# Optimization experiments

Hardware: AMD Instinct MI355X
Metric: run time of the kernel (lower is better)

## Reference

```python
import jax, jax.numpy as jnp
import numpy as np

FEATURE_DIM = 128
VALUE_DIM = 128


def setup_inputs() -> dict:
    key = jax.random.key(0)
    k1, k2, k3 = jax.random.split(key, 3)
    BH, S = 32, 4096
    q = jax.random.normal(k1, (BH, S, FEATURE_DIM), dtype=jnp.float32)
    k = jax.random.normal(k2, (BH, S, FEATURE_DIM), dtype=jnp.float32)
    v = jax.random.normal(k3, (BH, S, VALUE_DIM), dtype=jnp.float32)
    return {"q": q, "k": k, "v": v, "chunk_size": 128}


def reference(q, k, v, chunk_size):
    # q,k: [BH,S,F]; v: [BH,S,V]. Chunked fast-weight linear-attention scan:
    # out_t = q_t . (sum_{s<=t} k_s (x) v_s) / t
    BH, S, F = q.shape
    V = v.shape[-1]
    C = max(1, int(chunk_size))
    assert S % C == 0, "seq_len must be divisible by chunk_size for this reference"
    n_chunks = S // C
    # [n_chunks, BH, C, dim] for lax.scan over chunks
    qc = q.reshape(BH, n_chunks, C, F).transpose(1, 0, 2, 3)
    kc = k.reshape(BH, n_chunks, C, F).transpose(1, 0, 2, 3)
    vc = v.reshape(BH, n_chunks, C, V).transpose(1, 0, 2, 3)

    w0 = jnp.zeros((BH, F, V), dtype=q.dtype)

    def step(w_state, inputs):
        qi, ki, vi = inputs  # [BH,C,F], [BH,C,F], [BH,C,V]
        kv = jnp.einsum('bnf,bnv->bnfv', ki, vi)          # [BH,C,F,V]
        w_prefix = jnp.cumsum(kv, axis=1) + w_state[:, None]  # inclusive prefix sums
        out = jnp.einsum('bnf,bnfv->bnv', qi, w_prefix)    # [BH,C,V]
        return w_prefix[:, -1], out

    _, outs = jax.lax.scan(step, w0, (qc, kc, vc))
    out = outs.transpose(1, 0, 2, 3).reshape(BH, S, V)
    inv_counts = 1.0 / jnp.arange(1, S + 1, dtype=q.dtype)
    return out * inv_counts[None, :, None]
```

## Files before the change

kernel.cpp:

```cpp
#include <hip/hip_runtime.h>


typedef _Float16 f16;
typedef __attribute__((ext_vector_type(4))) _Float16 f16x4;
typedef __attribute__((ext_vector_type(8))) _Float16 f16x8;
typedef __attribute__((ext_vector_type(4))) float f32x4;
typedef __attribute__((ext_vector_type(16))) float f32x16;
typedef __attribute__((ext_vector_type(4))) float fv4;

#define MFMA16(a, b, c) __builtin_amdgcn_mfma_f32_16x16x32_f16((a), (b), (c), 0, 0, 0)
#define MFMA32(a, b, c) __builtin_amdgcn_mfma_f32_32x32x16_f16((a), (b), (c), 0, 0, 0)

__device__ __forceinline__ int swzb(int row, int col) {
  int s = (row ^ (row >> 3)) & 7;
  return (row << 8) + ((col << 1) ^ (s << 4));
}

__device__ __forceinline__ f16x8 frag32(const f16* lds, int row, int kk, int lane) {
  int c0 = (kk << 4) + ((lane >> 5) << 3);
  return *(const f16x8*)((const char*)lds + swzb(row, c0));
}

__device__ __forceinline__ int rowf(int r, int g) {
  return (r & 3) + ((r >> 2) << 3) + (g << 2);
}

__global__ __launch_bounds__(512, 1)
void ttr_pt(const float* __restrict__ k, const float* __restrict__ v,
            f16* __restrict__ pt) {
  __shared__ f16 kT[128 * 128];
  __shared__ f16 vT[128 * 128];
  const int tid = threadIdx.x, lane = tid & 63, wave = tid >> 6;
  const int bh = blockIdx.x >> 5, c = blockIdx.x & 31;
  const float* kg = k + ((size_t)bh * 4096 + c * 128) * 128;
  const float* vg = v + ((size_t)bh * 4096 + c * 128) * 128;
  const int f0 = (tid & 31) << 2;
#pragma unroll
  for (int p = 0; p < 8; ++p) {
    int s = (p << 4) + (tid >> 5);
    fv4 xk = *(const fv4*)(kg + s * 128 + f0);
    fv4 xv = *(const fv4*)(vg + s * 128 + f0);
#pragma unroll
    for (int e = 0; e < 4; ++e) {
      *(f16*)((char*)kT + swzb(f0 + e, s)) = (f16)xk[e];
      *(f16*)((char*)vT + swzb(f0 + e, s)) = (f16)xv[e];
    }
  }
  __syncthreads();
  const int l31 = lane & 31, g = lane >> 5;
  const int mt = wave >> 1, nt0 = (wave & 1) << 1;
  f32x16 p0 = {0.f}, p1 = {0.f};
#pragma unroll
  for (int kk = 0; kk < 8; ++kk) {
    f16x8 a = frag32(vT, (mt << 5) + l31, kk, lane);
    p0 = MFMA32(a, frag32(kT, (nt0 << 5) + l31, kk, lane), p0);
    p1 = MFMA32(a, frag32(kT, ((nt0 + 1) << 5) + l31, kk, lane), p1);
  }
  f16* dst = pt + (size_t)blockIdx.x * 16384;
#pragma unroll
  for (int r = 0; r < 16; ++r) {
    int vr = (mt << 5) + rowf(r, g);
    dst[vr * 128 + (nt0 << 5) + l31] = (f16)p0[r];
    dst[vr * 128 + ((nt0 + 1) << 5) + l31] = (f16)p1[r];
  }
}

__global__ __launch_bounds__(256, 1)
void ttr_prefix(const f16* __restrict__ pt, f16* __restrict__ w) {
  __shared__ f16 xch[256 * 8];
  const int tid = threadIdx.x;
  const int bh = blockIdx.x >> 3, vs = blockIdx.x & 7;
  const int v0 = vs << 4;
  const int NT = v0 >> 5;
  const int vloc = tid >> 4, fblk = tid & 15;
  const size_t bhbase = (size_t)bh * 32 * 16384;
  const f16* src = pt + bhbase + (size_t)(v0 + vloc) * 128 + fblk * 8;
  const int kk = tid >> 5, gg = (tid >> 4) & 1, lc = tid & 15;
  f16* dstu = w + bhbase +
              (size_t)(((NT * 8 + kk) * 64) + gg * 32 + (v0 & 31) + lc) * 8;
  const int phi_w = vloc * 16 + (fblk ^ vloc);
  const int phi_r = lc * 16 + ((tid >> 4) ^ lc);
  float acc[8];
#pragma unroll
  for (int e = 0; e < 8; ++e) acc[e] = 0.f;
  for (int c = 0; c < 32; ++c) {
    f16x8 pcur = *(const f16x8*)(src + (size_t)c * 16384);
    f16x8 h;
#pragma unroll
    for (int e = 0; e < 8; ++e) h[e] = (f16)acc[e];
    *(f16x8*)(xch + phi_w * 8) = h;
    __syncthreads();
    f16x8 o = *(const f16x8*)(xch + phi_r * 8);
    *(f16x8*)(dstu + (size_t)c * 16384) = o;
    __syncthreads();
#pragma unroll
    for (int e = 0; e < 8; ++e) acc[e] += (float)pcur[e];
  }
}

__global__ __launch_bounds__(256, 1)
void ttr_out(const float* __restrict__ q, const float* __restrict__ k,
             const float* __restrict__ v, const f16* __restrict__ w,
             float* __restrict__ out) {
  __shared__ f16 q_lds[128 * 128];
  __shared__ f16 s_lds[128 * 128];
  __shared__ f16 vT[64 * 128];
  const int tid = threadIdx.x, lane = tid & 63, wave = tid >> 6;
  const int l31 = lane & 31, g = lane >> 5;
  const int vhalf = blockIdx.x >> 10;
  const int bhc = blockIdx.x & 1023;
  const int bh = bhc >> 5, c = bhc & 31;
  const float* qg = q + ((size_t)bh * 4096 + c * 128) * 128;
  const float* kg = k + ((size_t)bh * 4096 + c * 128) * 128;
  const float* vg = v + ((size_t)bh * 4096 + c * 128) * 128 + vhalf * 64;

  const f16* wb = w + (size_t)bhc * 16384;
  f16x8 wf0[8], wf1[8];
#pragma unroll
  for (int kk = 0; kk < 8; ++kk) {
    int NT = vhalf * 2;
    wf0[kk] = *(const f16x8*)(wb + (size_t)(((NT * 8 + kk) * 64) + lane) * 8);
    wf1[kk] = *(const f16x8*)(wb + (size_t)((((NT + 1) * 8 + kk) * 64) + lane) * 8);
  }
  const int f0 = (tid & 31) << 2;
#pragma unroll
  for (int p = 0; p < 16; ++p) {
    int s = (p << 3) + (tid >> 5);
    fv4 xq = *(const fv4*)(qg + s * 128 + f0);
    f16x4 hq = {(f16)xq[0], (f16)xq[1], (f16)xq[2], (f16)xq[3]};
    *(f16x4*)((char*)q_lds + swzb(s, f0)) = hq;
    fv4 xk = *(const fv4*)(kg + s * 128 + f0);
    f16x4 hk = {(f16)xk[0], (f16)xk[1], (f16)xk[2], (f16)xk[3]};
    *(f16x4*)((char*)s_lds + swzb(s, f0)) = hk;
  }
  const int c0 = (tid & 15) << 2;
#pragma unroll
  for (int p = 0; p < 8; ++p) {
    int s = (p << 4) + (tid >> 4);
    fv4 xv = *(const fv4*)(vg + s * 128 + c0);
#pragma unroll
    for (int e = 0; e < 4; ++e)
      *(f16*)((char*)vT + swzb(c0 + e, s)) = (f16)xv[e];
  }
  __syncthreads();

  int mts[3], jts[3], ntiles;
  switch (wave) {
    case 0:  mts[0]=0; jts[0]=0; mts[1]=2; jts[1]=1; mts[2]=3; jts[2]=2; ntiles=3; break;
    case 1:  mts[0]=1; jts[0]=0; mts[1]=2; jts[1]=2; mts[2]=3; jts[2]=3; ntiles=3; break;
    case 2:  mts[0]=1; jts[0]=1; mts[1]=3; jts[1]=0; mts[2]=0; jts[2]=0; ntiles=2; break;
    default: mts[0]=2; jts[0]=0; mts[1]=3; jts[1]=1; mts[2]=0; jts[2]=0; ntiles=2; break;
  }
  f32x16 sa0 = {0.f}, sa1 = {0.f}, sa2 = {0.f};
  f32x16 o0 = {0.f}, o1 = {0.f};
#pragma unroll
  for (int kk = 0; kk < 8; ++kk) {
    sa0 = MFMA32(frag32(q_lds, (mts[0] << 5) + l31, kk, lane),
                 frag32(s_lds, (jts[0] << 5) + l31, kk, lane), sa0);
    sa1 = MFMA32(frag32(q_lds, (mts[1] << 5) + l31, kk, lane),
                 frag32(s_lds, (jts[1] << 5) + l31, kk, lane), sa1);
    if (ntiles == 3)
      sa2 = MFMA32(frag32(q_lds, (mts[2] << 5) + l31, kk, lane),
                   frag32(s_lds, (jts[2] << 5) + l31, kk, lane), sa2);
    f16x8 aq = frag32(q_lds, (wave << 5) + l31, kk, lane);
    o0 = MFMA32(aq, wf0[kk], o0);
    o1 = MFMA32(aq, wf1[kk], o1);
  }
  __syncthreads();

#define STORE_S(ACC, MT, JT)                                                  \
  {                                                                           \
    const bool dg = ((MT) == (JT));                                           \
    _Pragma("unroll") for (int r = 0; r < 16; ++r) {                          \
      int rl = rowf(r, g);                                                    \
      float val = ACC[r];                                                     \
      if (dg && l31 > rl) val = 0.f;                                          \
      *(f16*)((char*)s_lds + swzb(((MT) << 5) + rl, ((JT) << 5) + l31)) =     \
          (f16)val;                                                           \
    }                                                                         \
  }
  STORE_S(sa0, mts[0], jts[0]);
  STORE_S(sa1, mts[1], jts[1]);
  if (ntiles == 3) STORE_S(sa2, mts[2], jts[2]);
  __syncthreads();

  const int nkk = (wave + 1) << 1;
  for (int kk = 0; kk < nkk; ++kk) {
    f16x8 as = frag32(s_lds, (wave << 5) + l31, kk, lane);
    o0 = MFMA32(as, frag32(vT, l31, kk, lane), o0);
    o1 = MFMA32(as, frag32(vT, 32 + l31, kk, lane), o1);
  }
  float* og = out + (((size_t)bh * 4096) + c * 128 + (wave << 5)) * 128 + vhalf * 64;
#pragma unroll
  for (int r = 0; r < 16; ++r) {
    int rl = rowf(r, g);
    float tg = (float)(c * 128 + (wave << 5) + rl + 1);
    og[rl * 128 + l31] = o0[r] / tg;
    og[rl * 128 + 32 + l31] = o1[r] / tg;
  }
}

__device__ __forceinline__ f16x8 fragr(const f16* lds, int row, int kbase, int lane) {
  int c0 = kbase + ((lane >> 4) << 3);
  return *(const f16x8*)((const char*)lds + swzb(row, c0));
}
__device__ __forceinline__ f16x8 fragkT(const f16* lds, int kbase, int col, int lane) {
  f16x8 r;
  int r0 = kbase + ((lane >> 4) << 3);
#pragma unroll
  for (int j = 0; j < 8; ++j)
    r[j] = *(const f16*)((const char*)lds + swzb(r0 + j, col));
  return r;
}

__global__ __launch_bounds__(512, 1)
void ttr_fastweight(const float* __restrict__ q, const float* __restrict__ k,
                    const float* __restrict__ v, float* __restrict__ out) {
  __shared__ f16 q_lds[128 * 128];
  __shared__ f16 k_lds[128 * 128];
  __shared__ f16 a_lds[128 * 128];
  __shared__ f16 vT_lds[16 * 128];
  __shared__ f16 wT_lds[2][16 * 128];
  const int tid = threadIdx.x;
  const int lane = tid & 63;
  const int wave = tid >> 6;
  const int vg = blockIdx.x >> 5;
  const int b = blockIdx.x & 31;
  const float* qb = q + (size_t)b * (4096 * 128);
  const float* kb = k + (size_t)b * (4096 * 128);
  const float* vb = v + (size_t)b * (4096 * 128) + vg * 16;
  float* ob = out + (size_t)b * (4096 * 128) + vg * 16;
  for (int i = tid; i < 16 * 128; i += 512) wT_lds[0][i] = (f16)0.f;
  f32x4 wacc = {0.f, 0.f, 0.f, 0.f};
  __syncthreads();
  const int colj = lane & 15;
  const int row4 = (lane >> 4) << 2;
  for (int chunk = 0; chunk < 32; ++chunk) {
    const int cur = chunk & 1, nxt = cur ^ 1;
    __syncthreads();
    {
      const float* qg = qb + (size_t)chunk * (128 * 128);
      const float* kg = kb + (size_t)chunk * (128 * 128);
      int rr = tid >> 5;
      int cc = (tid & 31) << 2;
#pragma unroll
      for (int p = 0; p < 8; ++p) {
        int row = (p << 4) + rr;
        fv4 x = *(const fv4*)(qg + row * 128 + cc);
        f16x4 h = {(f16)x[0], (f16)x[1], (f16)x[2], (f16)x[3]};
        *(f16x4*)((char*)q_lds + swzb(row, cc)) = h;
        fv4 y = *(const fv4*)(kg + row * 128 + cc);
        f16x4 h2 = {(f16)y[0], (f16)y[1], (f16)y[2], (f16)y[3]};
        *(f16x4*)((char*)k_lds + swzb(row, cc)) = h2;
      }
      const float* vgp = vb + (size_t)chunk * (128 * 128);
      int vrow = tid >> 2;
      int vp = (tid & 3) << 2;
      fv4 xv = *(const fv4*)(vgp + vrow * 128 + vp);
#pragma unroll
      for (int t = 0; t < 4; ++t)
        *(f16*)((char*)vT_lds + swzb(vp + t, vrow)) = (f16)xv[t];
    }
    __syncthreads();
    {
      int u = 0;
      for (int r = 0; r < 8; ++r) {
        for (int c2 = 0; c2 <= r; ++c2) {
          if ((u++ & 7) != wave) continue;
          f32x4 acc = {0.f, 0.f, 0.f, 0.f};
          int arow = (r << 4) + colj;
          int brow = (c2 << 4) + colj;
#pragma unroll
          for (int kk = 0; kk < 4; ++kk)
            acc = MFMA16(fragr(q_lds, arow, kk << 5, lane),
                         fragr(k_lds, brow, kk << 5, lane), acc);
#pragma unroll
          for (int t = 0; t < 4; ++t) {
            float val = acc[t];
            if (r == c2 && colj > row4 + t) val = 0.f;
            *(f16*)((char*)a_lds + swzb((r << 4) + row4 + t, (c2 << 4) + colj)) =
                (f16)val;
          }
        }
      }
      if (wave < 4) {
        int r = wave << 1;
#pragma unroll
        for (int t = 0; t < 4; ++t)
          *(f16*)((char*)a_lds +
                  swzb((r << 4) + row4 + t, ((r + 1) << 4) + colj)) = (f16)0.f;
      }
#pragma unroll
      for (int kk = 0; kk < 4; ++kk)
        wacc = MFMA16(fragr(vT_lds, colj, kk << 5, lane),
                      fragkT(k_lds, kk << 5, (wave << 4) + colj, lane), wacc);
#pragma unroll
      for (int t = 0; t < 4; ++t)
        *(f16*)((char*)wT_lds[nxt] + swzb(row4 + t, (wave << 4) + colj)) =
            (f16)wacc[t];
    }
    __syncthreads();
    {
      int r = wave;
      int qrow = (r << 4) + colj;
      f32x4 acc = {0.f, 0.f, 0.f, 0.f};
#pragma unroll
      for (int kk = 0; kk < 4; ++kk)
        acc = MFMA16(fragr(q_lds, qrow, kk << 5, lane),
                     fragr(wT_lds[cur], colj, kk << 5, lane), acc);
      int nkk = (r + 2) >> 1;
      for (int kk = 0; kk < nkk; ++kk)
        acc = MFMA16(fragr(a_lds, qrow, kk << 5, lane),
                     fragr(vT_lds, colj, kk << 5, lane), acc);
      float* og = ob + (size_t)((chunk << 7) + (r << 4)) * 128 + colj;
#pragma unroll
      for (int t = 0; t < 4; ++t) {
        int lr = row4 + t;
        float tg = (float)((chunk << 7) + (r << 4) + lr + 1);
        og[(size_t)lr * 128] = acc[t] / tg;
      }
    }
  }
}

extern "C" void kernel_launch(void* const* d_in, const int* in_sizes, int n_in,
                              void* d_out, int out_size, void* d_ws, size_t ws_size,
                              hipStream_t stream) {
  const float* q = (const float*)d_in[0];
  const float* k = (const float*)d_in[1];
  const float* v = (const float*)d_in[2];
  float* o = (float*)d_out;
  const size_t need = (size_t)2 * 32 * 32 * 16384 * sizeof(f16);
  if (ws_size >= need) {
    f16* pt = (f16*)d_ws;
    f16* w = pt + (size_t)32 * 32 * 16384;
    ttr_pt<<<dim3(1024), dim3(512), 0, stream>>>(k, v, pt);
    ttr_prefix<<<dim3(256), dim3(256), 0, stream>>>(pt, w);
    ttr_out<<<dim3(2048), dim3(256), 0, stream>>>(q, k, v, w, o);
  } else {
    ttr_fastweight<<<dim3(256), dim3(512), 0, stream>>>(q, k, v, o);
  }
}
```

Baseline: 112.5 us.

## Split output kernel into V-quarters with Q fragments in registers

The output kernel now splits the value dimension into four 32-wide slices instead of two 64-wide halves, giving twice as many blocks. Each wave loads its own Q rows directly from global into registers, so the Q LDS tile goes away. Each wave computes only its own row strip of the causal QK^T, which removes one barrier, and launch bounds now allow three blocks per CU. The fallback single-kernel path and the workspace-size check are removed. In exchange, K and the QK^T product are loaded and computed again for every V slice, which doubles that redundant work and K traffic.

Result: slower. 135.0 us (+20.0%).

```diff
diff --git a/kernel.cpp b/kernel.cpp
--- a/kernel.cpp
+++ b/kernel.cpp
@@ -98,228 +98,103 @@
   }
 }
 
-__global__ __launch_bounds__(256, 1)
+__global__ __launch_bounds__(256, 3)
 void ttr_out(const float* __restrict__ q, const float* __restrict__ k,
              const float* __restrict__ v, const f16* __restrict__ w,
              float* __restrict__ out) {
-  __shared__ f16 q_lds[128 * 128];
   __shared__ f16 s_lds[128 * 128];
-  __shared__ f16 vT[64 * 128];
+  __shared__ f16 vT[32 * 128];
   const int tid = threadIdx.x, lane = tid & 63, wave = tid >> 6;
   const int l31 = lane & 31, g = lane >> 5;
-  const int vhalf = blockIdx.x >> 10;
-  const int bhc = blockIdx.x & 1023;
-  const int bh = bhc >> 5, c = bhc & 31;
+  const int widx = blockIdx.x & 31;
+  const int gidx = ((blockIdx.x >> 5) << 3) + (widx & 7);
+  const int vq = widx >> 3;
+  const int bh = gidx >> 5, c = gidx & 31;
   const float* qg = q + ((size_t)bh * 4096 + c * 128) * 128;
   const float* kg = k + ((size_t)bh * 4096 + c * 128) * 128;
-  const float* vg = v + ((size_t)bh * 4096 + c * 128) * 128 + vhalf * 64;
-
-  const f16* wb = w + (size_t)bhc * 16384;
-  f16x8 wf0[8], wf1[8];
+  const float* vg = v + ((size_t)bh * 4096 + c * 128) * 128 + vq * 32;
+
+  const f16* wb = w + (size_t)gidx * 16384;
+  f16x8 wf[8];
+#pragma unroll
+  for (int kk = 0; kk < 8; ++kk)
+    wf[kk] = *(const f16x8*)(wb + (size_t)(((vq * 8 + kk) * 64) + lane) * 8);
+
+  f16x8 qf[8];
+  {
+    const float* qr = qg + ((wave << 5) + l31) * 128 + (g << 3);
+#pragma unroll
+    for (int kk = 0; kk < 8; ++kk) {
+      fv4 a = *(const fv4*)(qr + (kk << 4));
+      fv4 b = *(const fv4*)(qr + (kk << 4) + 4);
+      f16x8 h = {(f16)a[0], (f16)a[1], (f16)a[2], (f16)a[3],
+                 (f16)b[0], (f16)b[1], (f16)b[2], (f16)b[3]};
+      qf[kk] = h;
+    }
+  }
+
+  {
+    const int c0 = (tid & 31) << 2;
+#pragma unroll
+    for (int p = 0; p < 16; ++p) {
+      int s = (p << 3) + (tid >> 5);
+      fv4 xk = *(const fv4*)(kg + s * 128 + c0);
+      f16x4 hk = {(f16)xk[0], (f16)xk[1], (f16)xk[2], (f16)xk[3]};
+      *(f16x4*)((char*)s_lds + swzb(s, c0)) = hk;
+    }
+  }
+  {
+    const int c0 = (tid & 7) << 2;
+#pragma unroll
+    for (int p = 0; p < 4; ++p) {
+      int s = (p << 5) + (tid >> 3);
+      fv4 xv = *(const fv4*)(vg + s * 128 + c0);
+#pragma unroll
+      for (int e = 0; e < 4; ++e)
+        *(f16*)((char*)vT + swzb(c0 + e, s)) = (f16)xv[e];
+    }
+  }
+  __syncthreads();
+
+  f32x16 s0 = {0.f}, s1 = {0.f}, s2 = {0.f}, s3 = {0.f}, o0 = {0.f};
 #pragma unroll
   for (int kk = 0; kk < 8; ++kk) {
-    int NT = vhalf * 2;
-    wf0[kk] = *(const f16x8*)(wb + (size_t)(((NT * 8 + kk) * 64) + lane) * 8);
-    wf1[kk] = *(const f16x8*)(wb + (size_t)((((NT + 1) * 8 + kk) * 64) + lane) * 8);
-  }
-  const int f0 = (tid & 31) << 2;
-#pragma unroll
-  for (int p = 0; p < 16; ++p) {
-    int s = (p << 3) + (tid >> 5);
-    fv4 xq = *(const fv4*)(qg + s * 128 + f0);
-    f16x4 hq = {(f16)xq[0], (f16)xq[1], (f16)xq[2], (f16)xq[3]};
-    *(f16x4*)((char*)q_lds + swzb(s, f0)) = hq;
-    fv4 xk = *(const fv4*)(kg + s * 128 + f0);
-    f16x4 hk = {(f16)xk[0], (f16)xk[1], (f16)xk[2], (f16)xk[3]};
-    *(f16x4*)((char*)s_lds + swzb(s, f0)) = hk;
-  }
-  const int c0 = (tid & 15) << 2;
-#pragma unroll
-  for (int p = 0; p < 8; ++p) {
-    int s = (p << 4) + (tid >> 4);
-    fv4 xv = *(const fv4*)(vg + s * 128 + c0);
-#pragma unroll
-    for (int e = 0; e < 4; ++e)
-      *(f16*)((char*)vT + swzb(c0 + e, s)) = (f16)xv[e];
+    f16x8 aq = qf[kk];
+    o0 = MFMA32(aq, wf[kk], o0);
+    s0 = MFMA32(aq, frag32(s_lds, l31, kk, lane), s0);
+    if (wave >= 1) s1 = MFMA32(aq, frag32(s_lds, 32 + l31, kk, lane), s1);
+    if (wave >= 2) s2 = MFMA32(aq, frag32(s_lds, 64 + l31, kk, lane), s2);
+    if (wave >= 3) s3 = MFMA32(aq, frag32(s_lds, 96 + l31, kk, lane), s3);
   }
   __syncthreads();
 
-  int mts[3], jts[3], ntiles;
-  switch (wave) {
-    case 0:  mts[0]=0; jts[0]=0; mts[1]=2; jts[1]=1; mts[2]=3; jts[2]=2; ntiles=3; break;
-    case 1:  mts[0]=1; jts[0]=0; mts[1]=2; jts[1]=2; mts[2]=3; jts[2]=3; ntiles=3; break;
-    case 2:  mts[0]=1; jts[0]=1; mts[1]=3; jts[1]=0; mts[2]=0; jts[2]=0; ntiles=2; break;
-    default: mts[0]=2; jts[0]=0; mts[1]=3; jts[1]=1; mts[2]=0; jts[2]=0; ntiles=2; break;
-  }
-  f32x16 sa0 = {0.f}, sa1 = {0.f}, sa2 = {0.f};
-  f32x16 o0 = {0.f}, o1 = {0.f};
-#pragma unroll
-  for (int kk = 0; kk < 8; ++kk) {
-    sa0 = MFMA32(frag32(q_lds, (mts[0] << 5) + l31, kk, lane),
-                 frag32(s_lds, (jts[0] << 5) + l31, kk, lane), sa0);
-    sa1 = MFMA32(frag32(q_lds, (mts[1] << 5) + l31, kk, lane),
-                 frag32(s_lds, (jts[1] << 5) + l31, kk, lane), sa1);
-    if (ntiles == 3)
-      sa2 = MFMA32(frag32(q_lds, (mts[2] << 5) + l31, kk, lane),
-                   frag32(s_lds, (jts[2] << 5) + l31, kk, lane), sa2);
-    f16x8 aq = frag32(q_lds, (wave << 5) + l31, kk, lane);
-    o0 = MFMA32(aq, wf0[kk], o0);
-    o1 = MFMA32(aq, wf1[kk], o1);
-  }
-  __syncthreads();
-
-#define STORE_S(ACC, MT, JT)                                                  \
+#define STORE_S(ACC, J)                                                       \
   {                                                                           \
-    const bool dg = ((MT) == (JT));                                           \
+    const bool dg = ((J) == wave);                                            \
     _Pragma("unroll") for (int r = 0; r < 16; ++r) {                          \
       int rl = rowf(r, g);                                                    \
       float val = ACC[r];                                                     \
       if (dg && l31 > rl) val = 0.f;                                          \
-      *(f16*)((char*)s_lds + swzb(((MT) << 5) + rl, ((JT) << 5) + l31)) =     \
+      *(f16*)((char*)s_lds + swzb((wave << 5) + rl, ((J) << 5) + l31)) =      \
           (f16)val;                                                           \
     }                                                                         \
   }
-  STORE_S(sa0, mts[0], jts[0]);
-  STORE_S(sa1, mts[1], jts[1]);
-  if (ntiles == 3) STORE_S(sa2, mts[2], jts[2]);
-  __syncthreads();
+  STORE_S(s0, 0);
+  if (wave >= 1) STORE_S(s1, 1);
+  if (wave >= 2) STORE_S(s2, 2);
+  if (wave >= 3) STORE_S(s3, 3);
 
   const int nkk = (wave + 1) << 1;
-  for (int kk = 0; kk < nkk; ++kk) {
-    f16x8 as = frag32(s_lds, (wave << 5) + l31, kk, lane);
-    o0 = MFMA32(as, frag32(vT, l31, kk, lane), o0);
-    o1 = MFMA32(as, frag32(vT, 32 + l31, kk, lane), o1);
-  }
-  float* og = out + (((size_t)bh * 4096) + c * 128 + (wave << 5)) * 128 + vhalf * 64;
+  for (int kk = 0; kk < nkk; ++kk)
+    o0 = MFMA32(frag32(s_lds, (wave << 5) + l31, kk, lane),
+                frag32(vT, l31, kk, lane), o0);
+
+  float* og = out + (((size_t)bh * 4096) + c * 128 + (wave << 5)) * 128 + vq * 32;
 #pragma unroll
   for (int r = 0; r < 16; ++r) {
     int rl = rowf(r, g);
     float tg = (float)(c * 128 + (wave << 5) + rl + 1);
     og[rl * 128 + l31] = o0[r] / tg;
-    og[rl * 128 + 32 + l31] = o1[r] / tg;
-  }
-}
-
-__device__ __forceinline__ f16x8 fragr(const f16* lds, int row, int kbase, int lane) {
-  int c0 = kbase + ((lane >> 4) << 3);
-  return *(const f16x8*)((const char*)lds + swzb(row, c0));
-}
-__device__ __forceinline__ f16x8 fragkT(const f16* lds, int kbase, int col, int lane) {
-  f16x8 r;
-  int r0 = kbase + ((lane >> 4) << 3);
-#pragma unroll
-  for (int j = 0; j < 8; ++j)
-    r[j] = *(const f16*)((const char*)lds + swzb(r0 + j, col));
-  return r;
-}
-
-__global__ __launch_bounds__(512, 1)
-void ttr_fastweight(const float* __restrict__ q, const float* __restrict__ k,
-                    const float* __restrict__ v, float* __restrict__ out) {
-  __shared__ f16 q_lds[128 * 128];
-  __shared__ f16 k_lds[128 * 128];
-  __shared__ f16 a_lds[128 * 128];
-  __shared__ f16 vT_lds[16 * 128];
-  __shared__ f16 wT_lds[2][16 * 128];
-  const int tid = threadIdx.x;
-  const int lane = tid & 63;
-  const int wave = tid >> 6;
-  const int vg = blockIdx.x >> 5;
-  const int b = blockIdx.x & 31;
-  const float* qb = q + (size_t)b * (4096 * 128);
-  const float* kb = k + (size_t)b * (4096 * 128);
-  const float* vb = v + (size_t)b * (4096 * 128) + vg * 16;
-  float* ob = out + (size_t)b * (4096 * 128) + vg * 16;
-  for (int i = tid; i < 16 * 128; i += 512) wT_lds[0][i] = (f16)0.f;
-  f32x4 wacc = {0.f, 0.f, 0.f, 0.f};
-  __syncthreads();
-  const int colj = lane & 15;
-  const int row4 = (lane >> 4) << 2;
-  for (int chunk = 0; chunk < 32; ++chunk) {
-    const int cur = chunk & 1, nxt = cur ^ 1;
-    __syncthreads();
-    {
-      const float* qg = qb + (size_t)chunk * (128 * 128);
-      const float* kg = kb + (size_t)chunk * (128 * 128);
-      int rr = tid >> 5;
-      int cc = (tid & 31) << 2;
-#pragma unroll
-      for (int p = 0; p < 8; ++p) {
-        int row = (p << 4) + rr;
-        fv4 x = *(const fv4*)(qg + row * 128 + cc);
-        f16x4 h = {(f16)x[0], (f16)x[1], (f16)x[2], (f16)x[3]};
-        *(f16x4*)((char*)q_lds + swzb(row, cc)) = h;
-        fv4 y = *(const fv4*)(kg + row * 128 + cc);
-        f16x4 h2 = {(f16)y[0], (f16)y[1], (f16)y[2], (f16)y[3]};
-        *(f16x4*)((char*)k_lds + swzb(row, cc)) = h2;
-      }
-      const float* vgp = vb + (size_t)chunk * (128 * 128);
-      int vrow = tid >> 2;
-      int vp = (tid & 3) << 2;
-      fv4 xv = *(const fv4*)(vgp + vrow * 128 + vp);
-#pragma unroll
-      for (int t = 0; t < 4; ++t)
-        *(f16*)((char*)vT_lds + swzb(vp + t, vrow)) = (f16)xv[t];
-    }
-    __syncthreads();
-    {
-      int u = 0;
-      for (int r = 0; r < 8; ++r) {
-        for (int c2 = 0; c2 <= r; ++c2) {
-          if ((u++ & 7) != wave) continue;
-          f32x4 acc = {0.f, 0.f, 0.f, 0.f};
-          int arow = (r << 4) + colj;
-          int brow = (c2 << 4) + colj;
-#pragma unroll
-          for (int kk = 0; kk < 4; ++kk)
-            acc = MFMA16(fragr(q_lds, arow, kk << 5, lane),
-                         fragr(k_lds, brow, kk << 5, lane), acc);
-#pragma unroll
-          for (int t = 0; t < 4; ++t) {
-            float val = acc[t];
-            if (r == c2 && colj > row4 + t) val = 0.f;
-            *(f16*)((char*)a_lds + swzb((r << 4) + row4 + t, (c2 << 4) + colj)) =
-                (f16)val;
-          }
-        }
-      }
-      if (wave < 4) {
-        int r = wave << 1;
-#pragma unroll
-        for (int t = 0; t < 4; ++t)
-          *(f16*)((char*)a_lds +
-                  swzb((r << 4) + row4 + t, ((r + 1) << 4) + colj)) = (f16)0.f;
-      }
-#pragma unroll
-      for (int kk = 0; kk < 4; ++kk)
-        wacc = MFMA16(fragr(vT_lds, colj, kk << 5, lane),
-                      fragkT(k_lds, kk << 5, (wave << 4) + colj, lane), wacc);
-#pragma unroll
-      for (int t = 0; t < 4; ++t)
-        *(f16*)((char*)wT_lds[nxt] + swzb(row4 + t, (wave << 4) + colj)) =
-            (f16)wacc[t];
-    }
-    __syncthreads();
-    {
-      int r = wave;
-      int qrow = (r << 4) + colj;
-      f32x4 acc = {0.f, 0.f, 0.f, 0.f};
-#pragma unroll
-      for (int kk = 0; kk < 4; ++kk)
-        acc = MFMA16(fragr(q_lds, qrow, kk << 5, lane),
-                     fragr(wT_lds[cur], colj, kk << 5, lane), acc);
-      int nkk = (r + 2) >> 1;
-      for (int kk = 0; kk < nkk; ++kk)
-        acc = MFMA16(fragr(a_lds, qrow, kk << 5, lane),
-                     fragr(vT_lds, colj, kk << 5, lane), acc);
-      float* og = ob + (size_t)((chunk << 7) + (r << 4)) * 128 + colj;
-#pragma unroll
-      for (int t = 0; t < 4; ++t) {
-        int lr = row4 + t;
-        float tg = (float)((chunk << 7) + (r << 4) + lr + 1);
-        og[(size_t)lr * 128] = acc[t] / tg;
-      }
-    }
   }
 }
 
@@ -330,14 +205,9 @@
   const float* k = (const float*)d_in[1];
   const float* v = (const float*)d_in[2];
   float* o = (float*)d_out;
-  const size_t need = (size_t)2 * 32 * 32 * 16384 * sizeof(f16);
-  if (ws_size >= need) {
-    f16* pt = (f16*)d_ws;
-    f16* w = pt + (size_t)32 * 32 * 16384;
-    ttr_pt<<<dim3(1024), dim3(512), 0, stream>>>(k, v, pt);
-    ttr_prefix<<<dim3(256), dim3(256), 0, stream>>>(pt, w);
-    ttr_out<<<dim3(2048), dim3(256), 0, stream>>>(q, k, v, w, o);
-  } else {
-    ttr_fastweight<<<dim3(256), dim3(512), 0, stream>>>(q, k, v, o);
-  }
-}
+  f16* pt = (f16*)d_ws;
+  f16* w = pt + (size_t)32 * 32 * 16384;
+  ttr_pt<<<dim3(1024), dim3(512), 0, stream>>>(k, v, pt);
+  ttr_prefix<<<dim3(256), dim3(256), 0, stream>>>(pt, w);
+  ttr_out<<<dim3(4096), dim3(256), 0, stream>>>(q, k, v, w, o);
+}
```
